# Kernel optimization log

Hardware: AMD Instinct MI355X
Metric: run time of the kernel (lower is better)

The kernel has to match this reference:

```python
import jax, jax.numpy as jnp
import numpy as np

N_GENE, N_TRAIN, E = 2500, 16384, 4194304
SRC_DIM, DST_DIM, HID, OUT, NCLS = 2500, 2675, 2500, 2500, 16


def setup_inputs() -> dict:
    key = jax.random.key(0)
    ks = jax.random.split(key, 16)
    s = 0.02
    return {
        "gene_feat": jax.random.normal(ks[0], (N_GENE, SRC_DIM), jnp.float32),
        "train_feat": jax.random.normal(ks[1], (N_TRAIN, DST_DIM), jnp.float32),
        "edge_src": jax.random.randint(ks[2], (E,), 0, N_GENE, jnp.int32),
        "edge_dst": jax.random.randint(ks[3], (E,), 0, N_TRAIN, jnp.int32),
        # conv1: SAGEConv((src=2500, dst=2675) -> 2500, mean)
        "W1_self": jax.random.normal(ks[4], (HID, DST_DIM), jnp.float32) * s,
        "W1_neigh": jax.random.normal(ks[5], (HID, SRC_DIM), jnp.float32) * s,
        "b1": jnp.zeros((HID,), jnp.float32),
        # conv2: SAGEConv(2500 -> 2500, mean); src feats are original gene feats
        "W2_self": jax.random.normal(ks[6], (OUT, HID), jnp.float32) * s,
        "W2_neigh": jax.random.normal(ks[7], (OUT, SRC_DIM), jnp.float32) * s,
        "b2": jnp.zeros((OUT,), jnp.float32),
        # classifier MLP
        "Wc1": jax.random.normal(ks[8], (OUT, OUT), jnp.float32) * s,
        "bc1": jnp.zeros((OUT,), jnp.float32),
        "Wc2": jax.random.normal(ks[9], (NCLS, OUT), jnp.float32) * s,
        "bc2": jnp.zeros((NCLS,), jnp.float32),
    }


def reference(gene_feat, train_feat, edge_src, edge_dst,
              W1_self, W1_neigh, b1, W2_self, W2_neigh, b2,
              Wc1, bc1, Wc2, bc2):
    # Dense incidence-count matrix A[dst, src]: # edges between (dst, src).
    # mean-aggregation over in-edges == (A @ gene_feat) / in_degree.
    A = jnp.zeros((N_TRAIN, N_GENE), jnp.float32).at[edge_dst, edge_src].add(1.0)
    deg = jnp.maximum(A.sum(axis=1, keepdims=True), 1.0)  # zero-in-deg -> neigh term = 0
    mean_src = (A @ gene_feat) / deg                      # [N_train, 2500]

    # conv1 ('connects'): fc_self(dst) + fc_neigh(mean(src)) + bias; then ReLU
    h = jax.nn.relu(train_feat @ W1_self.T + mean_src @ W1_neigh.T + b1)

    # conv2: dst feats = h, src feats = original gene_feat (same graph)
    h2 = jax.nn.relu(h @ W2_self.T + mean_src @ W2_neigh.T + b2)

    # classifier MLP
    return jax.nn.relu(h2 @ Wc1.T + bc1) @ Wc2.T + bc2   # [N_train, 16]
```

## Files before the change

### kernel.cpp

```cpp
#include <hip/hip_runtime.h>
#include <stdint.h>

typedef unsigned short u16;
typedef unsigned int u32;
typedef __attribute__((ext_vector_type(4))) float f32x4;
typedef __attribute__((ext_vector_type(8))) short bf16x8;

#define MROWS 16384
#define NP    2560
#define K1P   2688


__device__ __forceinline__ u16 f2bf(float f) {
    u32 u = __float_as_uint(f);
    u32 r = (u + 0x7fffu + ((u >> 16) & 1u)) >> 16;
    return (u16)r;
}

__device__ __forceinline__ void async_ld16(const void* g, void* l) {
    __builtin_amdgcn_global_load_lds((const __attribute__((address_space(1))) u32*)g,
                                     (__attribute__((address_space(3))) u32*)l,
                                     16, 0, 0);
}

__device__ __forceinline__ u32 lds_b(const void* p) {
    return (u32)(uintptr_t)(const __attribute__((address_space(3))) void*)p;
}


__global__ void cvt_pad(const float* __restrict__ src, u16* __restrict__ dst,
                        int R, int C, int Cp) {
    const int r = blockIdx.x;
    u16* drow = dst + (size_t)r * Cp;
    if (r < R) {
        const float* srow = src + (size_t)r * C;
        for (int c = threadIdx.x; c < Cp; c += blockDim.x)
            drow[c] = (c < C) ? f2bf(srow[c]) : (u16)0;
    } else {
        for (int c = threadIdx.x; c < Cp; c += blockDim.x) drow[c] = 0;
    }
}

__global__ void pad_vec(const float* __restrict__ src, float* __restrict__ dst,
                        int n, int np) {
    int i = blockIdx.x * blockDim.x + threadIdx.x;
    if (i < np) dst[i] = (i < n) ? src[i] : 0.f;
}

__global__ void transpose_cvt(const float* __restrict__ src, u16* __restrict__ dst) {
    __shared__ float t[64][65];
    const int n0 = blockIdx.x * 64;
    const int k0 = blockIdx.y * 64;
    const int tx = threadIdx.x, ty = threadIdx.y;
    for (int i = ty; i < 64; i += 4) {
        int k = k0 + i, n = n0 + tx;
        t[i][tx] = (k < 2500 && n < 2500) ? src[(size_t)k * 2500 + n] : 0.f;
    }
    __syncthreads();
    for (int i = ty; i < 64; i += 4)
        dst[(size_t)(n0 + i) * NP + k0 + tx] = f2bf(t[tx][i]);
}

__global__ void build_counts(const int* __restrict__ esrc, const int* __restrict__ edst,
                             int E, float* __restrict__ acnt) {
    int i = blockIdx.x * blockDim.x + threadIdx.x;
    if (i < E) atomicAdd(&acnt[(size_t)edst[i] * NP + esrc[i]], 1.0f);
}

__global__ void row_rdeg(const float* __restrict__ acnt, float* __restrict__ rdeg) {
    const int row = blockIdx.x;
    const float4* p = (const float4*)(acnt + (size_t)row * NP);
    float s = 0.f;
    for (int i = threadIdx.x; i < NP / 4; i += 64) {
        float4 v = p[i];
        s += v.x + v.y + v.z + v.w;
    }
    #pragma unroll
    for (int off = 32; off > 0; off >>= 1) s += __shfl_down(s, off, 64);
    if (threadIdx.x == 0) rdeg[row] = 1.f / fmaxf(s, 1.f);
}


#define DSR(dst, ad, off) \
    asm volatile("ds_read_b128 %0, %1 offset:%2" : "=v"(dst) : "v"(ad), "i"(off))

#define RD_A(SET, BUF, QM) do { \
    DSR(SET[0][0], adA0, (BUF)*32768 + (QM)*8192 + 0);    \
    DSR(SET[0][1], adA1, (BUF)*32768 + (QM)*8192 + 0);    \
    DSR(SET[1][0], adA0, (BUF)*32768 + (QM)*8192 + 2048); \
    DSR(SET[1][1], adA1, (BUF)*32768 + (QM)*8192 + 2048); \
    DSR(SET[2][0], adA0, (BUF)*32768 + (QM)*8192 + 4096); \
    DSR(SET[2][1], adA1, (BUF)*32768 + (QM)*8192 + 4096); \
    DSR(SET[3][0], adA0, (BUF)*32768 + (QM)*8192 + 6144); \
    DSR(SET[3][1], adA1, (BUF)*32768 + (QM)*8192 + 6144); \
} while (0)

#define RD_B01(BUF) do { \
    DSR(b[0][0], adB0, (BUF)*32768 + 0);    \
    DSR(b[0][1], adB1, (BUF)*32768 + 0);    \
    DSR(b[1][0], adB0, (BUF)*32768 + 2048); \
    DSR(b[1][1], adB1, (BUF)*32768 + 2048); \
} while (0)

#define RD_B23(BUF) do { \
    DSR(b[2][0], adB0, (BUF)*32768 + 4096); \
    DSR(b[2][1], adB1, (BUF)*32768 + 4096); \
    DSR(b[3][0], adB0, (BUF)*32768 + 6144); \
    DSR(b[3][1], adB1, (BUF)*32768 + 6144); \
} while (0)

#define WAITLG(N) do { \
    asm volatile("s_waitcnt lgkmcnt(" #N ")" ::: "memory"); \
    __builtin_amdgcn_sched_barrier(0); \
} while (0)

#define MFMA_Q(QM, QN, ASET) do { \
    __builtin_amdgcn_s_setprio(1); \
    _Pragma("unroll") \
    for (int mi_ = 0; mi_ < 4; ++mi_) { \
        _Pragma("unroll") \
        for (int ni_ = 0; ni_ < 2; ++ni_) { \
            f32x4 c_ = acc[(QM)*4 + mi_][(QN)*2 + ni_]; \
            c_ = __builtin_amdgcn_mfma_f32_16x16x32_bf16(ASET[mi_][0], b[(QN)*2 + ni_][0], c_, 0, 0, 0); \
            c_ = __builtin_amdgcn_mfma_f32_16x16x32_bf16(ASET[mi_][1], b[(QN)*2 + ni_][1], c_, 0, 0, 0); \
            acc[(QM)*4 + mi_][(QN)*2 + ni_] = c_; \
        } \
    } \
    __builtin_amdgcn_s_setprio(0); \
} while (0)

#define XFEN() asm volatile("" ::: "memory")
#define XBAR() do { XFEN(); __builtin_amdgcn_s_barrier(); XFEN(); } while (0)
#define WVM6() asm volatile("s_waitcnt vmcnt(6)" ::: "memory")

template<bool PAIR2, bool BIAS_RELU>
__global__ __launch_bounds__(512, 2) void gemm256(
    const u16* __restrict__ A1, const u16* __restrict__ B1, int K1,
    const u16* __restrict__ A2, const u16* __restrict__ B2, int K2,
    const float* __restrict__ epi, u16* __restrict__ C, int N)
{
    __shared__ __align__(16) u16 lA[2 * 256 * 64];
    __shared__ __align__(16) u16 lB[2 * 256 * 64];

    const int tid  = threadIdx.x;
    const int nwg  = gridDim.x;
    const int orig = blockIdx.x;
    const int swz  = (orig & 7) * (nwg >> 3) + (orig >> 3);
    const int nt   = N >> 8;
    const int bm   = (swz / nt) << 8;
    const int bn   = (swz % nt) << 8;

    const int wave = tid >> 6, lane = tid & 63;
    const int wr   = (wave >> 2) << 7;
    const int wc   = (wave & 3) << 6;
    const int lrow = lane & 15, lkq = (lane >> 4) & 3;
    const int o0   = ((lkq ^ (lrow & 7)) << 3);

    const u32 adA0 = lds_b(lA + (wr + lrow) * 64 + o0);
    const u32 adA1 = adA0 ^ 64;
    const u32 adB0 = lds_b(lB + (wc + lrow) * 64 + o0);
    const u32 adB1 = adB0 ^ 64;

    const int sr   = tid >> 3;
    const int pc   = tid & 7;
    const int swzc = ((pc ^ (sr & 7)) << 3);
    u16* const dA  = lA + sr * 64 + pc * 8;
    u16* const dB  = lB + sr * 64 + pc * 8;

    const int nk1 = K1 >> 6;
    const int nkt = nk1 + (PAIR2 ? (K2 >> 6) : 0);

    f32x4 acc[8][4] = {};
    bf16x8 a1[4][2], a2[4][2], b[4][2];

    auto STAGE = [&](int mat, int buf, int half, int kt) {
        int v = (kt < nkt) ? kt : kt - nkt;
        const u16* base; int K, ko;
        if (!PAIR2 || v < nk1) { base = mat ? B1 : A1; K = K1; ko = v << 6; }
        else                   { base = mat ? B2 : A2; K = K2; ko = (v - nk1) << 6; }
        const int rb = (mat ? bn : bm) + (half << 7) + sr;
        u16* d = (mat ? dB : dA) + buf * 16384 + half * 8192;
        const u16* g = base + (size_t)rb * K + ko + swzc;
        async_ld16(g, d);
        async_ld16(g + (size_t)64 * K, d + 4096);
    };

    STAGE(1, 0, 0, 0); STAGE(1, 0, 1, 0); STAGE(0, 0, 0, 0); STAGE(0, 0, 1, 0);
    STAGE(1, 1, 0, 1); STAGE(1, 1, 1, 1); STAGE(0, 1, 0, 1);
    WVM6();
    XBAR();
    RD_A(a1, 0, 0);

    const int niter = nkt >> 1;
    #pragma unroll 1
    for (int i = 0; i < niter; ++i) {
        const int t1 = 2 * i + 1, t2 = 2 * i + 2, t3 = 2 * i + 3;
        RD_B01(0); RD_B23(0); STAGE(0, 1, 1, t1);
        XBAR(); WAITLG(0); MFMA_Q(0, 0, a1); XBAR();
        RD_A(a2, 0, 1); STAGE(1, 0, 0, t2);
        XBAR(); WAITLG(8); MFMA_Q(0, 1, a1); XBAR();
        STAGE(1, 0, 1, t2);
        XBAR(); WAITLG(0); MFMA_Q(1, 1, a2); XBAR();
        STAGE(0, 0, 0, t2); WVM6();
        XBAR(); RD_A(a1, 1, 0); WAITLG(8); MFMA_Q(1, 0, a2); XBAR();
        RD_B01(1); RD_B23(1); STAGE(0, 0, 1, t2);
        XBAR(); WAITLG(0); MFMA_Q(0, 0, a1); XBAR();
        RD_A(a2, 1, 1); STAGE(1, 1, 0, t3);
        XBAR(); WAITLG(8); MFMA_Q(0, 1, a1); XBAR();
        STAGE(1, 1, 1, t3);
        XBAR(); WAITLG(0); MFMA_Q(1, 1, a2); XBAR();
        STAGE(0, 1, 0, t3); WVM6();
        XBAR(); RD_A(a1, 0, 0); WAITLG(8); MFMA_Q(1, 0, a2); XBAR();
    }
    asm volatile("s_waitcnt vmcnt(0) lgkmcnt(0)" ::: "memory");

    const int rbase = bm + wr + lkq * 4;
    const int cbase = bn + wc + lrow;
    if (BIAS_RELU) {
        #pragma unroll
        for (int ni = 0; ni < 4; ++ni) {
            const float bv = epi[cbase + ni * 16];
            #pragma unroll
            for (int mi = 0; mi < 8; ++mi)
                #pragma unroll
                for (int r = 0; r < 4; ++r) {
                    float v = acc[mi][ni][r] + bv;
                    v = fmaxf(v, 0.f);
                    C[(size_t)(rbase + mi * 16 + r) * N + cbase + ni * 16] = f2bf(v);
                }
        }
    } else {
        #pragma unroll
        for (int mi = 0; mi < 8; ++mi)
            #pragma unroll
            for (int r = 0; r < 4; ++r) {
                const float sv = epi[rbase + mi * 16 + r];
                #pragma unroll
                for (int ni = 0; ni < 4; ++ni)
                    C[(size_t)(rbase + mi * 16 + r) * N + cbase + ni * 16] =
                        f2bf(acc[mi][ni][r] * sv);
            }
    }
}

__device__ __forceinline__ float bfdot2(u32 a, u32 b, float acc) {
    float al = __uint_as_float(a << 16), ah = __uint_as_float(a & 0xffff0000u);
    float bl = __uint_as_float(b << 16), bh = __uint_as_float(b & 0xffff0000u);
    return fmaf(ah, bh, fmaf(al, bl, acc));
}

__global__ __launch_bounds__(256) void gemm_cls(
    const u16* __restrict__ hc, const u16* __restrict__ Wc2,
    const float* __restrict__ bc2, float* __restrict__ out)
{
    const int c = threadIdx.x & 15;
    const int r = threadIdx.x >> 4;
    const int row = blockIdx.x * 16 + r;
    const uint4* hp = (const uint4*)(hc + (size_t)row * NP);
    const uint4* wp = (const uint4*)(Wc2 + (size_t)c * NP);
    float acc = 0.f;
    #pragma unroll 4
    for (int i = 0; i < NP / 8; ++i) {
        uint4 a = hp[i], b = wp[i];
        acc = bfdot2(a.x, b.x, acc);
        acc = bfdot2(a.y, b.y, acc);
        acc = bfdot2(a.z, b.z, acc);
        acc = bfdot2(a.w, b.w, acc);
    }
    out[(size_t)row * 16 + c] = acc + bc2[c];
}


extern "C" void kernel_launch(void* const* d_in, const int* in_sizes, int n_in,
                              void* d_out, int out_size, void* d_ws, size_t ws_size,
                              hipStream_t stream) {
    const float* gene  = (const float*)d_in[0];
    const float* train = (const float*)d_in[1];
    const int*   esrc  = (const int*)d_in[2];
    const int*   edst  = (const int*)d_in[3];
    const float* W1s   = (const float*)d_in[4];
    const float* W1n   = (const float*)d_in[5];
    const float* b1    = (const float*)d_in[6];
    const float* W2s   = (const float*)d_in[7];
    const float* W2n   = (const float*)d_in[8];
    const float* b2    = (const float*)d_in[9];
    const float* Wc1   = (const float*)d_in[10];
    const float* bc1   = (const float*)d_in[11];
    const float* Wc2   = (const float*)d_in[12];
    const float* bc2   = (const float*)d_in[13];
    const int E = in_sizes[2];

    char* ws = (char*)d_ws;
    const size_t o_acnt  = 0;
    const size_t o_acntb = 167772160;
    const size_t o_mean  = 251658240;
    const size_t o_train = 335544320;
    const size_t o_w1s   = 423624704;
    const size_t o_w1n   = 437387264;
    const size_t o_w2s   = 450494464;
    const size_t o_w2n   = 463601664;
    const size_t o_wc1   = 476708864;
    const size_t o_gft   = 489816064;
    const size_t o_wc2   = 502923264;
    const size_t o_b1    = 503005184;
    const size_t o_b2    = 503015424;
    const size_t o_bc1   = 503025664;
    const size_t o_rdeg  = 503035904;

    float* ACNT = (float*)(ws + o_acnt);
    u16* ACNTB  = (u16*)(ws + o_acntb);
    u16* MEAN   = (u16*)(ws + o_mean);
    u16* TRAINB = (u16*)(ws + o_train);
    u16* W1S    = (u16*)(ws + o_w1s);
    u16* W1N    = (u16*)(ws + o_w1n);
    u16* W2S    = (u16*)(ws + o_w2s);
    u16* W2N    = (u16*)(ws + o_w2n);
    u16* WC1    = (u16*)(ws + o_wc1);
    u16* GFT    = (u16*)(ws + o_gft);
    u16* WC2    = (u16*)(ws + o_wc2);
    float* B1   = (float*)(ws + o_b1);
    float* B2   = (float*)(ws + o_b2);
    float* BC1  = (float*)(ws + o_bc1);
    float* RDEG = (float*)(ws + o_rdeg);
    u16* H  = (u16*)(ws + o_acnt);
    u16* H2 = (u16*)(ws + o_acntb);
    u16* HC = (u16*)(ws + o_mean);

    hipMemsetAsync(ACNT, 0, (size_t)MROWS * NP * 4, stream);
    build_counts<<<(E + 255) / 256, 256, 0, stream>>>(esrc, edst, E, ACNT);
    row_rdeg<<<MROWS, 64, 0, stream>>>(ACNT, RDEG);

    cvt_pad<<<MROWS, 256, 0, stream>>>(ACNT, ACNTB, MROWS, NP, NP);
    cvt_pad<<<MROWS, 256, 0, stream>>>(train, TRAINB, MROWS, 2675, K1P);
    cvt_pad<<<NP, 256, 0, stream>>>(W1s, W1S, 2500, 2675, K1P);
    cvt_pad<<<NP, 256, 0, stream>>>(W1n, W1N, 2500, 2500, NP);
    cvt_pad<<<NP, 256, 0, stream>>>(W2s, W2S, 2500, 2500, NP);
    cvt_pad<<<NP, 256, 0, stream>>>(W2n, W2N, 2500, 2500, NP);
    cvt_pad<<<NP, 256, 0, stream>>>(Wc1, WC1, 2500, 2500, NP);
    cvt_pad<<<16, 256, 0, stream>>>(Wc2, WC2, 16, 2500, NP);
    transpose_cvt<<<dim3(NP / 64, NP / 64), dim3(64, 4), 0, stream>>>(gene, GFT);
    pad_vec<<<(NP + 255) / 256, 256, 0, stream>>>(b1, B1, 2500, NP);
    pad_vec<<<(NP + 255) / 256, 256, 0, stream>>>(b2, B2, 2500, NP);
    pad_vec<<<(NP + 255) / 256, 256, 0, stream>>>(bc1, BC1, 2500, NP);

    const int NWG = (NP / 256) * (MROWS / 256);
    gemm256<false, false><<<NWG, 512, 0, stream>>>(
        ACNTB, GFT, NP, nullptr, nullptr, 0, RDEG, MEAN, NP);
    gemm256<true, true><<<NWG, 512, 0, stream>>>(
        TRAINB, W1S, K1P, MEAN, W1N, NP, B1, H, NP);
    gemm256<true, true><<<NWG, 512, 0, stream>>>(
        H, W2S, NP, MEAN, W2N, NP, B2, H2, NP);
    gemm256<false, true><<<NWG, 512, 0, stream>>>(
        H2, WC1, NP, nullptr, nullptr, 0, BC1, HC, NP);
    gemm_cls<<<MROWS / 16, 256, 0, stream>>>(HC, WC2, bc2, (float*)d_out);
}
```

Baseline: 2.090 ms.

## Reschedule GEMM main loop to prefetch B fragments one quadrant ahead

Restructures the 256x256 bf16 GEMM inner loop so B-fragment LDS reads are split into halves and issued one MFMA quadrant ahead, using double-buffered B register sets. Each MFMA block now overlaps with the LDS reads for the next one, and the global-to-LDS staging order is changed so fewer async loads are in flight at each vmcnt wait. This aims to hide LDS read latency behind MFMA work. The cost is extra VGPRs for the additional B fragment sets under the 512-thread, 2-wave-per-SIMD launch bound, and the finer-grained wait counts add a risk of scheduling or correctness mistakes.

```diff
diff --git a/kernel.cpp b/kernel.cpp
--- a/kernel.cpp
+++ b/kernel.cpp
@@ -95,18 +95,11 @@
     DSR(SET[3][1], adA1, (BUF)*32768 + (QM)*8192 + 6144); \
 } while (0)
 
-#define RD_B01(BUF) do { \
-    DSR(b[0][0], adB0, (BUF)*32768 + 0);    \
-    DSR(b[0][1], adB1, (BUF)*32768 + 0);    \
-    DSR(b[1][0], adB0, (BUF)*32768 + 2048); \
-    DSR(b[1][1], adB1, (BUF)*32768 + 2048); \
-} while (0)
-
-#define RD_B23(BUF) do { \
-    DSR(b[2][0], adB0, (BUF)*32768 + 4096); \
-    DSR(b[2][1], adB1, (BUF)*32768 + 4096); \
-    DSR(b[3][0], adB0, (BUF)*32768 + 6144); \
-    DSR(b[3][1], adB1, (BUF)*32768 + 6144); \
+#define RD_BP(SET, BUF, BASE) do { \
+    DSR(SET[0][0], adB0, (BUF)*32768 + (BASE));        \
+    DSR(SET[0][1], adB1, (BUF)*32768 + (BASE));        \
+    DSR(SET[1][0], adB0, (BUF)*32768 + (BASE) + 2048); \
+    DSR(SET[1][1], adB1, (BUF)*32768 + (BASE) + 2048); \
 } while (0)
 
 #define WAITLG(N) do { \
@@ -114,15 +107,15 @@
     __builtin_amdgcn_sched_barrier(0); \
 } while (0)
 
-#define MFMA_Q(QM, QN, ASET) do { \
+#define MFMA_Q(QM, QN, ASET, BSET) do { \
     __builtin_amdgcn_s_setprio(1); \
     _Pragma("unroll") \
     for (int mi_ = 0; mi_ < 4; ++mi_) { \
         _Pragma("unroll") \
         for (int ni_ = 0; ni_ < 2; ++ni_) { \
             f32x4 c_ = acc[(QM)*4 + mi_][(QN)*2 + ni_]; \
-            c_ = __builtin_amdgcn_mfma_f32_16x16x32_bf16(ASET[mi_][0], b[(QN)*2 + ni_][0], c_, 0, 0, 0); \
-            c_ = __builtin_amdgcn_mfma_f32_16x16x32_bf16(ASET[mi_][1], b[(QN)*2 + ni_][1], c_, 0, 0, 0); \
+            c_ = __builtin_amdgcn_mfma_f32_16x16x32_bf16(ASET[mi_][0], BSET[ni_][0], c_, 0, 0, 0); \
+            c_ = __builtin_amdgcn_mfma_f32_16x16x32_bf16(ASET[mi_][1], BSET[ni_][1], c_, 0, 0, 0); \
             acc[(QM)*4 + mi_][(QN)*2 + ni_] = c_; \
         } \
     } \
@@ -131,7 +124,7 @@
 
 #define XFEN() asm volatile("" ::: "memory")
 #define XBAR() do { XFEN(); __builtin_amdgcn_s_barrier(); XFEN(); } while (0)
-#define WVM6() asm volatile("s_waitcnt vmcnt(6)" ::: "memory")
+#define WVM4() asm volatile("s_waitcnt vmcnt(4)" ::: "memory")
 
 template<bool PAIR2, bool BIAS_RELU>
 __global__ __launch_bounds__(512, 2) void gemm256(
@@ -171,7 +164,7 @@
     const int nkt = nk1 + (PAIR2 ? (K2 >> 6) : 0);
 
     f32x4 acc[8][4] = {};
-    bf16x8 a1[4][2], a2[4][2], b[4][2];
+    bf16x8 a1[4][2], a2[4][2], b23[2][2], b01A[2][2], b01B[2][2];
 
     auto STAGE = [&](int mat, int buf, int half, int kt) {
         int v = (kt < nkt) ? kt : kt - nkt;
@@ -185,32 +178,34 @@
         async_ld16(g + (size_t)64 * K, d + 4096);
     };
 
-    STAGE(1, 0, 0, 0); STAGE(1, 0, 1, 0); STAGE(0, 0, 0, 0); STAGE(0, 0, 1, 0);
-    STAGE(1, 1, 0, 1); STAGE(1, 1, 1, 1); STAGE(0, 1, 0, 1);
-    WVM6();
+    STAGE(1, 0, 0, 0); STAGE(1, 0, 1, 0);
+    STAGE(0, 0, 0, 0); STAGE(0, 0, 1, 0);
+    STAGE(1, 1, 0, 1); STAGE(1, 1, 1, 1);
+    WVM4();
     XBAR();
+    RD_BP(b01A, 0, 0);
     RD_A(a1, 0, 0);
 
     const int niter = nkt >> 1;
     #pragma unroll 1
     for (int i = 0; i < niter; ++i) {
         const int t1 = 2 * i + 1, t2 = 2 * i + 2, t3 = 2 * i + 3;
-        RD_B01(0); RD_B23(0); STAGE(0, 1, 1, t1);
-        XBAR(); WAITLG(0); MFMA_Q(0, 0, a1); XBAR();
-        RD_A(a2, 0, 1); STAGE(1, 0, 0, t2);
-        XBAR(); WAITLG(8); MFMA_Q(0, 1, a1); XBAR();
-        STAGE(1, 0, 1, t2);
-        XBAR(); WAITLG(0); MFMA_Q(1, 1, a2); XBAR();
-        STAGE(0, 0, 0, t2); WVM6();
-        XBAR(); RD_A(a1, 1, 0); WAITLG(8); MFMA_Q(1, 0, a2); XBAR();
-        RD_B01(1); RD_B23(1); STAGE(0, 0, 1, t2);
-        XBAR(); WAITLG(0); MFMA_Q(0, 0, a1); XBAR();
-        RD_A(a2, 1, 1); STAGE(1, 1, 0, t3);
-        XBAR(); WAITLG(8); MFMA_Q(0, 1, a1); XBAR();
-        STAGE(1, 1, 1, t3);
-        XBAR(); WAITLG(0); MFMA_Q(1, 1, a2); XBAR();
-        STAGE(0, 1, 0, t3); WVM6();
-        XBAR(); RD_A(a1, 0, 0); WAITLG(8); MFMA_Q(1, 0, a2); XBAR();
+        STAGE(0, 1, 0, t1);
+        XBAR(); RD_BP(b23, 0, 4096); WAITLG(4); MFMA_Q(0, 0, a1, b01A); XBAR();
+        STAGE(0, 1, 1, t1); WVM4();
+        XBAR(); RD_A(a2, 0, 1); WAITLG(8); MFMA_Q(0, 1, a1, b23); XBAR();
+        STAGE(1, 0, 0, t2);
+        XBAR(); RD_BP(b01B, 1, 0); WAITLG(4); MFMA_Q(1, 1, a2, b23); XBAR();
+        STAGE(1, 0, 1, t2); WVM4();
+        XBAR(); RD_A(a1, 1, 0); MFMA_Q(1, 0, a2, b01A); XBAR();
+        STAGE(0, 0, 0, t2);
+        XBAR(); RD_BP(b23, 1, 4096); WAITLG(4); MFMA_Q(0, 0, a1, b01B); XBAR();
+        STAGE(0, 0, 1, t2); WVM4();
+        XBAR(); RD_A(a2, 1, 1); WAITLG(8); MFMA_Q(0, 1, a1, b23); XBAR();
+        STAGE(1, 1, 0, t3);
+        XBAR(); RD_BP(b01A, 0, 0); WAITLG(4); MFMA_Q(1, 1, a2, b23); XBAR();
+        STAGE(1, 1, 1, t3); WVM4();
+        XBAR(); RD_A(a1, 0, 0); MFMA_Q(1, 0, a2, b01B); XBAR();
     }
     asm volatile("s_waitcnt vmcnt(0) lgkmcnt(0)" ::: "memory");
 
```

New measurement: 2.175 ms. 1.04x slower.
